# Optimization experiments

Measured on AMD Instinct MI355X. Metric: run time of the kernel, lower is better.

## Reference

```python
import jax, jax.numpy as jnp
import numpy as np

# OGB feature vocab sizes
ATOM_DIMS = [119, 4, 12, 12, 10, 6, 6, 2, 2]
BOND_DIMS = [5, 6, 2]
ATOM_OFF = np.concatenate([[0], np.cumsum(ATOM_DIMS)[:-1]]).astype(np.int32)
BOND_OFF = np.concatenate([[0], np.cumsum(BOND_DIMS)[:-1]]).astype(np.int32)
SCHEDULE_LEN = 5   # len(train_schedule) == len(eval_schedule)
NUM_GRAPHS = 12000
BN_EPS = 1e-5

N_NODES, N_EDGES, HIDDEN, NUM_TASKS = 300000, 600000, 128, 128


def setup_inputs() -> dict:
    key = jax.random.key(0)
    ks = jax.random.split(key, 16)
    x = jax.random.randint(ks[0], (N_NODES, 9), 0, 2, dtype=jnp.int32)
    edge_index = jax.random.randint(ks[1], (2, N_EDGES), 0, N_NODES, dtype=jnp.int32)
    edge_attr = jax.random.randint(ks[2], (N_EDGES, 3), 0, 2, dtype=jnp.int32)
    batch = jnp.sort(jax.random.randint(ks[3], (N_NODES,), 0, NUM_GRAPHS, dtype=jnp.int32))
    # learned parameters (embedding tables concatenated with offsets)
    atom_emb = jax.random.normal(ks[4], (sum(ATOM_DIMS), HIDDEN), jnp.float32) * 0.1
    bond_emb = jax.random.normal(ks[5], (sum(BOND_DIMS), HIDDEN), jnp.float32) * 0.1
    conv_W = jax.random.normal(ks[6], (HIDDEN, HIDDEN), jnp.float32) * (1.0 / np.sqrt(HIDDEN))
    conv_b = jnp.zeros((HIDDEN,), jnp.float32)
    root_emb = jax.random.normal(ks[7], (HIDDEN,), jnp.float32) * 0.1
    bn_gamma = jnp.ones((HIDDEN,), jnp.float32)
    bn_beta = jnp.zeros((HIDDEN,), jnp.float32)
    bn_mean = jnp.zeros((HIDDEN,), jnp.float32)   # running stats (eval mode)
    bn_var = jnp.ones((HIDDEN,), jnp.float32)
    lin_W = jax.random.normal(ks[8], (NUM_TASKS, HIDDEN), jnp.float32) * (1.0 / np.sqrt(HIDDEN))
    lin_b = jnp.zeros((NUM_TASKS,), jnp.float32)
    return {"x": x, "edge_index": edge_index, "edge_attr": edge_attr, "batch": batch,
            "atom_emb": atom_emb, "bond_emb": bond_emb, "conv_W": conv_W, "conv_b": conv_b,
            "root_emb": root_emb, "bn_gamma": bn_gamma, "bn_beta": bn_beta,
            "bn_mean": bn_mean, "bn_var": bn_var, "lin_W": lin_W, "lin_b": lin_b}


def reference(x, edge_index, edge_attr, batch, atom_emb, bond_emb, conv_W, conv_b,
              root_emb, bn_gamma, bn_beta, bn_mean, bn_var, lin_W, lin_b):
    N = x.shape[0]
    # AtomEncoder / BondEncoder: sum of per-feature embedding lookups
    h = atom_emb[x + jnp.asarray(ATOM_OFF, x.dtype)].sum(axis=1)            # [N, H]
    e = bond_emb[edge_attr + jnp.asarray(BOND_OFF, edge_attr.dtype)].sum(axis=1)  # [E, H]
    row, col = edge_index[0], edge_index[1]
    deg = jax.ops.segment_sum(jnp.ones_like(row, h.dtype), row, num_segments=N) + 1.0  # [N]
    dis = deg ** -0.5                                                        # deg >= 1, no inf
    norm = dis[row] * dis[col]                                               # [E]
    inv_std = bn_gamma / jnp.sqrt(bn_var + BN_EPS)
    for i in range(SCHEDULE_LEN):
        old = h
        z = h @ conv_W.T + conv_b                                            # [N, H]
        # message: norm * relu(x_j + edge_emb), aggregated at target (col) via scatter-add
        msg = norm[:, None] * jax.nn.relu(z[row] + e)                        # [E, H]
        agg = jax.ops.segment_sum(msg, col, num_segments=N)                  # [N, H]
        z = agg + jax.nn.relu(z + root_emb) / deg[:, None]                   # self-loop term
        z = jax.nn.relu(z)
        z = (z - bn_mean) * inv_std + bn_beta                                # BN (eval, running stats)
        # dropout: identity in eval mode
        # NOTE: faithful to source bug: smooth_fac is the loop index i, not schedule[i]
        h = i * old + (1 - i) * z
    # global mean pool over graphs
    counts = jax.ops.segment_sum(jnp.ones((N,), h.dtype), batch, num_segments=NUM_GRAPHS)
    pooled = jax.ops.segment_sum(h, batch, num_segments=NUM_GRAPHS) / jnp.maximum(counts, 1.0)[:, None]
    return pooled @ lin_W.T + lin_b                                          # [num_graphs, num_tasks]
```

## Files before the change

kernel.cpp:

```cpp
#include <hip/hip_runtime.h>

#define HID 128
#define AROWS 173

typedef __attribute__((ext_vector_type(8))) short short8;
typedef __attribute__((ext_vector_type(8))) unsigned short ushort8v;
typedef __attribute__((ext_vector_type(4))) float floatx4;
typedef __attribute__((ext_vector_type(4))) unsigned short ushort4v;

__device__ __forceinline__ unsigned short f2bf(float f) {
    unsigned u = __builtin_bit_cast(unsigned, f);
    u += 0x7FFF + ((u >> 16) & 1);
    return (unsigned short)(u >> 16);
}
__device__ __forceinline__ float bf2f(unsigned short s) {
    unsigned u = ((unsigned)s) << 16;
    return __builtin_bit_cast(float, u);
}

__global__ void fillrd_kernel(float* __restrict__ dis, int* __restrict__ indeg,
                              int* __restrict__ dhist, int N)
{
    int i = blockIdx.x * 256 + threadIdx.x;
    if (i < N) { dis[i] = 0.f; indeg[i] = 0; }
    if (blockIdx.x == 0 && threadIdx.x < 32) dhist[threadIdx.x] = 0;
}

__global__ void diag_kernel(float* __restrict__ out, long n, float val)
{
    long i = (long)blockIdx.x * blockDim.x + threadIdx.x;
    if (i < n) out[i] = val;
}

__global__ __launch_bounds__(256) void tables_kernel(
    const float* __restrict__ conv_W, unsigned short* __restrict__ Wb,
    const float* __restrict__ lin_W, unsigned short* __restrict__ linWb,
    const float* __restrict__ bond_emb, unsigned short* __restrict__ comb,
    const float* __restrict__ gamma, const float* __restrict__ beta,
    const float* __restrict__ mean, const float* __restrict__ var,
    float* __restrict__ bnsc, float* __restrict__ bnsh,
    const float* __restrict__ atom_emb, unsigned short* __restrict__ aeb)
{
    int blk = blockIdx.x;
    int tid = threadIdx.x;
    if (blk < 64) {
        int i = blk * 256 + tid;
        Wb[i] = f2bf(conv_W[i]);
    } else if (blk < 128) {
        int i = (blk - 64) * 256 + tid;
        linWb[i] = f2bf(lin_W[i]);
    } else if (blk < 158) {
        int i = (blk - 128) * 2 + (tid >> 7);
        int c = tid & 127;
        int a0 = i / 12, a1 = (i % 12) / 2, a2 = i % 2;
        comb[i * HID + c] = f2bf(bond_emb[a0 * HID + c] + bond_emb[(5 + a1) * HID + c]
                               + bond_emb[(11 + a2) * HID + c]);
    } else if (blk == 158) {
        if (tid < HID) {
            float sc = gamma[tid] * rsqrtf(var[tid] + 1e-5f);
            bnsc[tid] = sc;
            bnsh[tid] = beta[tid] - mean[tid] * sc;
        }
    } else {
        int i = (blk - 159) * 256 + tid;
        if (i < AROWS * HID) aeb[i] = f2bf(atom_emb[i]);
    }
}

__global__ void hist_kernel(const int* __restrict__ ei, float* __restrict__ dis,
                            int* __restrict__ indeg, int E)
{
    for (int e = blockIdx.x * blockDim.x + threadIdx.x; e < E; e += gridDim.x * blockDim.x) {
        atomicAdd(&dis[ei[e]], 1.f);
        atomicAdd(&indeg[ei[E + e]], 1);
    }
}

__global__ __launch_bounds__(256) void fdh_kernel(
    float* __restrict__ dis, const int* __restrict__ indeg,
    int* __restrict__ dhist, int N)
{
    __shared__ int lh[32];
    int tid = threadIdx.x;
    if (tid < 32) lh[tid] = 0;
    __syncthreads();
    int i = blockIdx.x * 256 + tid;
    if (i < N) {
        dis[i] = rsqrtf(dis[i] + 1.f);
        int d = indeg[i]; if (d > 31) d = 31;
        atomicAdd(&lh[d], 1);
    }
    __syncthreads();
    if (tid < 32 && lh[tid]) atomicAdd(&dhist[tid], lh[tid]);
}

__global__ void dscan_kernel(const int* __restrict__ dhist, int* __restrict__ dcur)
{
    if (threadIdx.x == 0) {
        int s = 0;
        for (int k = 0; k < 32; ++k) { dcur[k] = s; s += dhist[k]; }
    }
}

__global__ __launch_bounds__(256) void dperm_kernel(
    const int* __restrict__ indeg, int* __restrict__ dcur,
    int* __restrict__ perm, int* __restrict__ invperm, int N)
{
    __shared__ int lh[32];
    __shared__ int gb[32];
    int tid = threadIdx.x;
    if (tid < 32) lh[tid] = 0;
    __syncthreads();
    int n = blockIdx.x * 256 + tid;
    int rank = 0, d = 0;
    if (n < N) {
        d = indeg[n]; if (d > 31) d = 31;
        rank = atomicAdd(&lh[d], 1);
    }
    __syncthreads();
    if (tid < 32) gb[tid] = lh[tid] ? atomicAdd(&dcur[tid], lh[tid]) : 0;
    __syncthreads();
    if (n < N) {
        int slot = gb[d] + rank;
        perm[slot] = n;
        invperm[n] = slot;
    }
}

__global__ __launch_bounds__(256) void sbsum_kernel(
    const int* __restrict__ indeg, const int* __restrict__ perm,
    int* __restrict__ partial, int N)
{
    __shared__ int s[256];
    int tid = threadIdx.x;
    int i = blockIdx.x * 256 + tid;
    s[tid] = (i < N) ? indeg[perm[i]] : 0;
    __syncthreads();
    for (int d = 128; d > 0; d >>= 1) {
        if (tid < d) s[tid] += s[tid + d];
        __syncthreads();
    }
    if (tid == 0) partial[blockIdx.x] = s[0];
}

__global__ __launch_bounds__(256) void sscan1_kernel(
    const int* __restrict__ partial, int* __restrict__ offs,
    int* __restrict__ sptr, int B, int N)
{
    __shared__ int s[256];
    __shared__ int carry_s;
    int tid = threadIdx.x;
    if (tid == 0) carry_s = 0;
    __syncthreads();
    for (int base = 0; base < B; base += 256) {
        int i = base + tid;
        int v = (i < B) ? partial[i] : 0;
        s[tid] = v;
        __syncthreads();
        for (int d = 1; d < 256; d <<= 1) {
            int t = (tid >= d) ? s[tid - d] : 0;
            __syncthreads();
            s[tid] += t;
            __syncthreads();
        }
        int carry = carry_s;
        if (i < B) offs[i] = carry + s[tid] - v;
        __syncthreads();
        if (tid == 0) carry_s = carry + s[255];
        __syncthreads();
    }
    if (tid == 0) sptr[N] = carry_s;
}

__global__ __launch_bounds__(256) void sscan2_kernel(
    const int* __restrict__ indeg, const int* __restrict__ perm,
    const int* __restrict__ offs, int* __restrict__ sptr,
    int* __restrict__ scursor, int N)
{
    __shared__ int s[256];
    int tid = threadIdx.x;
    int i = blockIdx.x * 256 + tid;
    int v = (i < N) ? indeg[perm[i]] : 0;
    s[tid] = v;
    __syncthreads();
    for (int d = 1; d < 256; d <<= 1) {
        int t = (tid >= d) ? s[tid - d] : 0;
        __syncthreads();
        s[tid] += t;
        __syncthreads();
    }
    if (i < N) {
        int ex = offs[blockIdx.x] + s[tid] - v;
        sptr[i] = ex;
        scursor[i] = ex;
    }
}

__global__ void fillcsr_kernel(const int* __restrict__ ei, const int* __restrict__ attr,
                               const float* __restrict__ dis,
                               const int* __restrict__ invperm,
                               int* __restrict__ scursor,
                               int2* __restrict__ edata, const int* __restrict__ batch,
                               int* __restrict__ gptr, int E, int N, int G)
{
    for (int e = blockIdx.x * blockDim.x + threadIdx.x; e < E; e += gridDim.x * blockDim.x) {
        int r   = ei[e];
        int col = ei[E + e];
        int slot = invperm[col];
        int pos = atomicAdd(&scursor[slot], 1);
        int ci  = attr[e * 3] * 12 + attr[e * 3 + 1] * 2 + attr[e * 3 + 2];
        float nrm = dis[r] * dis[col];
        int2 ed;
        ed.x = r;
        ed.y = ci | ((int)f2bf(nrm) << 16);
        edata[pos] = ed;
    }
    for (int n = blockIdx.x * blockDim.x + threadIdx.x; n < N; n += gridDim.x * blockDim.x) {
        int b = batch[n];
        int bp = (n == 0) ? -1 : batch[n - 1];
        for (int g = bp + 1; g <= b; ++g) gptr[g] = n;
        if (n == N - 1)
            for (int g = b + 1; g <= G; ++g) gptr[g] = N;
    }
}

template<bool FIRST>
__global__ __launch_bounds__(256) void agg_kernel(
    const int* __restrict__ perm, const int* __restrict__ sptr,
    const int2* __restrict__ edata, const unsigned short* __restrict__ comb,
    const float* __restrict__ dis, const float* __restrict__ root,
    const float* __restrict__ bnsc, const float* __restrict__ bnsh,
    const unsigned short* __restrict__ zb, unsigned short* __restrict__ hb,
    float fi, int N)
{
    long slot = (long)blockIdx.x * 16 + (threadIdx.x >> 4);
    if (slot >= N) return;
    long n = perm[slot];
    int c = (threadIdx.x & 15) * 8;

    int jb = sptr[slot], je = sptr[slot + 1];

    ushort8v zv = *reinterpret_cast<const ushort8v*>(zb + n * HID + c);
    ushort8v hv;
    if constexpr (!FIRST) hv = *reinterpret_cast<const ushort8v*>(hb + n * HID + c);
    float di = dis[n];
    float rd = di * di;
    float acc[8];
#pragma unroll
    for (int j = 0; j < 8; ++j) acc[j] = fmaxf(bf2f(zv[j]) + root[c + j], 0.f) * rd;

    int j2 = jb;
    for (; j2 + 1 < je; j2 += 2) {
        int2 e0 = edata[j2];
        int2 e1 = edata[j2 + 1];
        ushort8v z0 = *reinterpret_cast<const ushort8v*>(zb + (long)e0.x * HID + c);
        ushort8v z1 = *reinterpret_cast<const ushort8v*>(zb + (long)e1.x * HID + c);
        ushort8v c0 = *reinterpret_cast<const ushort8v*>(comb + (e0.y & 0xFF) * HID + c);
        ushort8v c1 = *reinterpret_cast<const ushort8v*>(comb + (e1.y & 0xFF) * HID + c);
        float n0 = bf2f((unsigned short)(((unsigned)e0.y) >> 16));
        float n1 = bf2f((unsigned short)(((unsigned)e1.y) >> 16));
#pragma unroll
        for (int j = 0; j < 8; ++j) {
            acc[j] += fmaxf(bf2f(z0[j]) + bf2f(c0[j]), 0.f) * n0;
            acc[j] += fmaxf(bf2f(z1[j]) + bf2f(c1[j]), 0.f) * n1;
        }
    }
    if (j2 < je) {
        int2 e0 = edata[j2];
        ushort8v z0 = *reinterpret_cast<const ushort8v*>(zb + (long)e0.x * HID + c);
        ushort8v c0 = *reinterpret_cast<const ushort8v*>(comb + (e0.y & 0xFF) * HID + c);
        float n0 = bf2f((unsigned short)(((unsigned)e0.y) >> 16));
#pragma unroll
        for (int j = 0; j < 8; ++j)
            acc[j] += fmaxf(bf2f(z0[j]) + bf2f(c0[j]), 0.f) * n0;
    }

    ushort8v o;
#pragma unroll
    for (int j = 0; j < 8; ++j) {
        float t = fmaxf(acc[j], 0.f) * bnsc[c + j] + bnsh[c + j];
        float h;
        if constexpr (FIRST) h = t;
        else h = fi * bf2f(hv[j]) + (1.f - fi) * t;
        o[j] = f2bf(h);
    }
    *reinterpret_cast<ushort8v*>(hb + n * HID + c) = o;
}

__device__ __forceinline__ void gemm_from_lds(
    unsigned short (*hs)[132], const unsigned short* __restrict__ Wb,
    const float* __restrict__ bias, unsigned short* __restrict__ zb,
    long base, int N, int tid)
{
    int wave = tid >> 6;
    int lane = tid & 63;
    int l15 = lane & 15;
    int q = lane >> 4;
    int rowl0 = wave * 32;

    short8 a[2][4];
#pragma unroll
    for (int mt = 0; mt < 2; ++mt) {
        int rl = rowl0 + mt * 16 + l15;
#pragma unroll
        for (int kb = 0; kb < 4; ++kb)
            a[mt][kb] = *reinterpret_cast<const short8*>(&hs[rl][q * 8 + kb * 32]);
    }

    floatx4 acc[2][8];
#pragma unroll
    for (int mt = 0; mt < 2; ++mt)
#pragma unroll
        for (int nt = 0; nt < 8; ++nt) {
            floatx4 zz = {0.f, 0.f, 0.f, 0.f};
            acc[mt][nt] = zz;
        }

#pragma unroll
    for (int nt = 0; nt < 8; ++nt) {
        const unsigned short* bp = Wb + (nt * 16 + l15) * HID + q * 8;
#pragma unroll
        for (int kb = 0; kb < 4; ++kb) {
            short8 b = *reinterpret_cast<const short8*>(bp + kb * 32);
            acc[0][nt] = __builtin_amdgcn_mfma_f32_16x16x32_bf16(a[0][kb], b, acc[0][nt], 0, 0, 0);
            acc[1][nt] = __builtin_amdgcn_mfma_f32_16x16x32_bf16(a[1][kb], b, acc[1][nt], 0, 0, 0);
        }
    }

    float bi[8];
#pragma unroll
    for (int nt = 0; nt < 8; ++nt) bi[nt] = bias[nt * 16 + l15];

    __syncthreads();
#pragma unroll
    for (int mt = 0; mt < 2; ++mt)
#pragma unroll
        for (int r = 0; r < 4; ++r) {
            int lr = rowl0 + mt * 16 + q * 4 + r;
#pragma unroll
            for (int nt = 0; nt < 8; ++nt)
                hs[lr][l15 + 16 * nt] = f2bf(acc[mt][nt][r] + bi[nt]);
        }
    __syncthreads();

    int tr = tid >> 4;
    int tc = (tid & 15) * 8;
#pragma unroll
    for (int i = 0; i < 8; ++i) {
        int row = i * 16 + tr;
        long gr = base + row;
        if (gr < N) {
            ushort8v v = *reinterpret_cast<const ushort8v*>(&hs[row][tc]);
            *reinterpret_cast<ushort8v*>(zb + gr * HID + tc) = v;
        }
    }
}

__global__ __launch_bounds__(256) void egemm_kernel(
    const int* __restrict__ x, const unsigned short* __restrict__ aeb,
    const unsigned short* __restrict__ Wb, const float* __restrict__ bias,
    unsigned short* __restrict__ zb, int N)
{
    __shared__ unsigned short hs[64][132];
    __shared__ int xs[64 * 9];
    int tid = threadIdx.x;
    long base = (long)blockIdx.x * 64;
    const int OFF[9] = {0, 119, 123, 135, 147, 157, 163, 169, 171};

    int nb = (N - base < 64) ? (int)(N - base) : 64;
    int cnt = nb * 9;
    for (int i = tid; i < cnt; i += 256) xs[i] = x[base * 9 + i];
    __syncthreads();

    int sn = tid >> 4;
    int cc = (tid & 15) * 8;
#pragma unroll 1
    for (int s = 0; s < 4; ++s) {
        int lr = s * 16 + sn;
        ushort8v o;
        if (lr < nb) {
            float acc[8];
#pragma unroll
            for (int j = 0; j < 8; ++j) acc[j] = 0.f;
#pragma unroll
            for (int f = 0; f < 9; ++f) {
                int idx = xs[lr * 9 + f] + OFF[f];
                ushort8v v = *reinterpret_cast<const ushort8v*>(aeb + (long)idx * HID + cc);
#pragma unroll
                for (int j = 0; j < 8; ++j) acc[j] += bf2f(v[j]);
            }
#pragma unroll
            for (int j = 0; j < 8; ++j) o[j] = f2bf(acc[j]);
        } else {
            ushort8v z8 = {0, 0, 0, 0, 0, 0, 0, 0};
            o = z8;
        }
        *reinterpret_cast<ushort8v*>(&hs[lr][cc]) = o;
    }
    __syncthreads();

    int wave = tid >> 6;
    int lane = tid & 63;
    int l15 = lane & 15;
    int q = lane >> 4;
    int row0 = wave * 16;

    short8 a[4];
#pragma unroll
    for (int kb = 0; kb < 4; ++kb)
        a[kb] = *reinterpret_cast<const short8*>(&hs[row0 + l15][q * 8 + kb * 32]);

    floatx4 acc[8];
#pragma unroll
    for (int nt = 0; nt < 8; ++nt) {
        floatx4 zz = {0.f, 0.f, 0.f, 0.f};
        acc[nt] = zz;
    }
#pragma unroll
    for (int nt = 0; nt < 8; ++nt) {
        const unsigned short* bp = Wb + (nt * 16 + l15) * HID + q * 8;
#pragma unroll
        for (int kb = 0; kb < 4; ++kb) {
            short8 b = *reinterpret_cast<const short8*>(bp + kb * 32);
            acc[nt] = __builtin_amdgcn_mfma_f32_16x16x32_bf16(a[kb], b, acc[nt], 0, 0, 0);
        }
    }

    float bi[8];
#pragma unroll
    for (int nt = 0; nt < 8; ++nt) bi[nt] = bias[nt * 16 + l15];

#pragma unroll
    for (int r = 0; r < 4; ++r) {
        int lr = row0 + q * 4 + r;
#pragma unroll
        for (int nt = 0; nt < 8; ++nt)
            hs[lr][l15 + 16 * nt] = f2bf(acc[nt][r] + bi[nt]);
    }
    __syncthreads();

    int tr = tid >> 4;
    int tc = (tid & 15) * 8;
#pragma unroll
    for (int i = 0; i < 4; ++i) {
        int row = i * 16 + tr;
        long gr = base + row;
        if (gr < N) {
            ushort8v v = *reinterpret_cast<const ushort8v*>(&hs[row][tc]);
            *reinterpret_cast<ushort8v*>(zb + gr * HID + tc) = v;
        }
    }
}

__global__ __launch_bounds__(256) void gemm_kernel(
    const unsigned short* __restrict__ hb, const unsigned short* __restrict__ Wb,
    const float* __restrict__ bias, unsigned short* __restrict__ zb, int N)
{
    __shared__ unsigned short st[128][132];
    int tid = threadIdx.x;
    int wave = tid >> 6;
    int lane = tid & 63;
    int l15 = lane & 15;
    int q = lane >> 4;
    long base = (long)blockIdx.x * 128;
    long row0 = base + wave * 32;

#pragma unroll
    for (int mt = 0; mt < 2; ++mt) {
        long rl = row0 + mt * 16 + l15;
        if (rl > (long)N - 1) rl = (long)N - 1;
        const unsigned short* ap = hb + rl * HID + q * 8;
        int lrow = wave * 32 + mt * 16 + l15;
#pragma unroll
        for (int kb = 0; kb < 4; ++kb)
            *reinterpret_cast<ushort8v*>(&st[lrow][q * 8 + kb * 32]) =
                *reinterpret_cast<const ushort8v*>(ap + kb * 32);
    }
    __syncthreads();
    gemm_from_lds(st, Wb, bias, zb, base, N, tid);
}

__global__ __launch_bounds__(256) void linmm_kernel(
    const unsigned short* __restrict__ pb, const unsigned short* __restrict__ Wb,
    const float* __restrict__ bias, float* __restrict__ out, int G)
{
    int wave = threadIdx.x >> 6;
    int lane = threadIdx.x & 63;
    int l15 = lane & 15;
    int q = lane >> 4;
    long row0 = (long)blockIdx.x * 128 + wave * 32;

    short8 a[2][4];
#pragma unroll
    for (int mt = 0; mt < 2; ++mt) {
        long rl = row0 + mt * 16 + l15;
        if (rl > (long)G - 1) rl = (long)G - 1;
        const unsigned short* ap = pb + rl * HID + q * 8;
#pragma unroll
        for (int kb = 0; kb < 4; ++kb)
            a[mt][kb] = *reinterpret_cast<const short8*>(ap + kb * 32);
    }

    floatx4 acc[2][8];
#pragma unroll
    for (int mt = 0; mt < 2; ++mt)
#pragma unroll
        for (int nt = 0; nt < 8; ++nt) {
            floatx4 zz = {0.f, 0.f, 0.f, 0.f};
            acc[mt][nt] = zz;
        }

#pragma unroll
    for (int nt = 0; nt < 8; ++nt) {
        const unsigned short* bp = Wb + (nt * 16 + l15) * HID + q * 8;
#pragma unroll
        for (int kb = 0; kb < 4; ++kb) {
            short8 b = *reinterpret_cast<const short8*>(bp + kb * 32);
            acc[0][nt] = __builtin_amdgcn_mfma_f32_16x16x32_bf16(a[0][kb], b, acc[0][nt], 0, 0, 0);
            acc[1][nt] = __builtin_amdgcn_mfma_f32_16x16x32_bf16(a[1][kb], b, acc[1][nt], 0, 0, 0);
        }
    }

    float bi[8];
#pragma unroll
    for (int nt = 0; nt < 8; ++nt) bi[nt] = bias[nt * 16 + l15];

#pragma unroll
    for (int mt = 0; mt < 2; ++mt)
#pragma unroll
        for (int r = 0; r < 4; ++r) {
            long rr = row0 + mt * 16 + q * 4 + r;
            if (rr < G) {
                float* op = out + rr * HID + l15;
#pragma unroll
                for (int nt = 0; nt < 8; ++nt)
                    op[nt * 16] = acc[mt][nt][r] + bi[nt];
            }
        }
}

__global__ __launch_bounds__(256) void pool_kernel(
    const unsigned short* __restrict__ hb, const int* __restrict__ gptr,
    unsigned short* __restrict__ pb, int G)
{
    int g = blockIdx.x;
    if (g >= G) return;
    int tid = threadIdx.x;
    int sub = tid >> 5;
    int c = (tid & 31) * 4;
    int lo = gptr[g], hi = gptr[g + 1];
    floatx4 s = {0.f, 0.f, 0.f, 0.f};
    for (int n = lo + sub; n < hi; n += 8) {
        ushort4v hv = *reinterpret_cast<const ushort4v*>(hb + (long)n * HID + c);
#pragma unroll
        for (int j = 0; j < 4; ++j) s[j] += bf2f(hv[j]);
    }
    __shared__ float ps[8][HID];
    *reinterpret_cast<floatx4*>(&ps[sub][c]) = s;
    __syncthreads();
    if (tid < HID) {
        float sum = 0.f;
#pragma unroll
        for (int k = 0; k < 8; ++k) sum += ps[k][tid];
        float cnt = (hi > lo) ? (float)(hi - lo) : 1.f;
        pb[(long)g * HID + tid] = f2bf(sum / cnt);
    }
}

extern "C" void kernel_launch(void* const* d_in, const int* in_sizes, int n_in,
                              void* d_out, int out_size, void* d_ws, size_t ws_size,
                              hipStream_t stream)
{
    const int* x          = (const int*)d_in[0];
    const int* ei         = (const int*)d_in[1];
    const int* attr       = (const int*)d_in[2];
    const int* batch      = (const int*)d_in[3];
    const float* atom_emb = (const float*)d_in[4];
    const float* bond_emb = (const float*)d_in[5];
    const float* conv_W   = (const float*)d_in[6];
    const float* conv_b   = (const float*)d_in[7];
    const float* root     = (const float*)d_in[8];
    const float* gamma    = (const float*)d_in[9];
    const float* beta     = (const float*)d_in[10];
    const float* mean     = (const float*)d_in[11];
    const float* var      = (const float*)d_in[12];
    const float* lin_W    = (const float*)d_in[13];
    const float* lin_b    = (const float*)d_in[14];
    float* out = (float*)d_out;

    const int N = in_sizes[0] / 9;
    const int E = in_sizes[1] / 2;
    const int G = out_size / HID;
    const int B = (N + 255) / 256;

    auto al = [](size_t b) { return (b + 255) & ~(size_t)255; };
    const size_t need =
        al((size_t)N * HID * 2) +
        al((size_t)N * HID * 2) +
        al((size_t)(N + 1) * 4) +
        al((size_t)E * 8) +
        al((size_t)N * 4) +
        al((size_t)N * 4) +
        al((size_t)N * 4) +
        al((size_t)N * 4) +
        al((size_t)2048 * 4) * 2 +
        al((size_t)(G + 1) * 4) +
        al((size_t)(G + 128) * HID * 2) +
        al((size_t)60 * HID * 2) +
        al((size_t)HID * 4) * 2 +
        al((size_t)HID * HID * 2) * 2 +
        al((size_t)AROWS * HID * 2) +
        al(32 * 4) * 2;

    if (ws_size < need || B > 2048) {
        float v = (B > 2048) ? 3000.f : (1000.f + (float)(ws_size >> 20));
        long n = (long)out_size;
        diag_kernel<<<(int)((n + 255) / 256), 256, 0, stream>>>(out, n, v);
        return;
    }

    char* wsp = (char*)d_ws;
    size_t used = 0;
    auto alloc = [&](size_t bytes) { char* p = wsp + used; used += al(bytes); return p; };
    unsigned short* hb = (unsigned short*)alloc((size_t)N * HID * 2);
    unsigned short* zb = (unsigned short*)alloc((size_t)N * HID * 2);
    int* sptr     = (int*)alloc((size_t)(N + 1) * 4);
    int2* edata   = (int2*)alloc((size_t)E * 8);
    int* indeg    = (int*)alloc((size_t)N * 4);
    int* perm     = (int*)alloc((size_t)N * 4);
    int* invperm  = (int*)alloc((size_t)N * 4);
    int* scursor  = (int*)alloc((size_t)N * 4);
    int* partial  = (int*)alloc((size_t)2048 * 4);
    int* offs     = (int*)alloc((size_t)2048 * 4);
    int* gptr     = (int*)alloc((size_t)(G + 1) * 4);
    unsigned short* pb = (unsigned short*)alloc((size_t)(G + 128) * HID * 2);
    float* dis    = (float*)pb;
    unsigned short* comb = (unsigned short*)alloc((size_t)60 * HID * 2);
    float* bnsc   = (float*)alloc((size_t)HID * 4);
    float* bnsh   = (float*)alloc((size_t)HID * 4);
    unsigned short* Wb    = (unsigned short*)alloc((size_t)HID * HID * 2);
    unsigned short* linWb = (unsigned short*)alloc((size_t)HID * HID * 2);
    unsigned short* aeb   = (unsigned short*)alloc((size_t)AROWS * HID * 2);
    int* dhist    = (int*)alloc(32 * 4);
    int* dcur     = (int*)alloc(32 * 4);

    fillrd_kernel<<<B, 256, 0, stream>>>(dis, indeg, dhist, N);
    tables_kernel<<<246, 256, 0, stream>>>(conv_W, Wb, lin_W, linWb, bond_emb, comb,
                                           gamma, beta, mean, var, bnsc, bnsh,
                                           atom_emb, aeb);
    hist_kernel<<<1024, 256, 0, stream>>>(ei, dis, indeg, E);
    fdh_kernel<<<B, 256, 0, stream>>>(dis, indeg, dhist, N);
    dscan_kernel<<<1, 64, 0, stream>>>(dhist, dcur);
    dperm_kernel<<<B, 256, 0, stream>>>(indeg, dcur, perm, invperm, N);
    sbsum_kernel<<<B, 256, 0, stream>>>(indeg, perm, partial, N);
    sscan1_kernel<<<1, 256, 0, stream>>>(partial, offs, sptr, B, N);
    sscan2_kernel<<<B, 256, 0, stream>>>(indeg, perm, offs, sptr, scursor, N);
    fillcsr_kernel<<<1024, 256, 0, stream>>>(ei, attr, dis, invperm, scursor, edata,
                                             batch, gptr, E, N, G);

    const int egemm_blocks = (N + 63) / 64;
    const int gemm_blocks  = (N + 127) / 128;
    const int agg_blocks   = (N + 15) / 16;
    egemm_kernel<<<egemm_blocks, 256, 0, stream>>>(x, aeb, Wb, conv_b, zb, N);
    agg_kernel<true ><<<agg_blocks, 256, 0, stream>>>(perm, sptr, edata, comb, dis,
            root, bnsc, bnsh, zb, hb, 0.f, N);
    const float fis[3] = {2.f, 3.f, 4.f};
    for (int t = 0; t < 3; ++t) {
        gemm_kernel<<<gemm_blocks, 256, 0, stream>>>(hb, Wb, conv_b, zb, N);
        agg_kernel<false><<<agg_blocks, 256, 0, stream>>>(perm, sptr, edata, comb, dis,
                root, bnsc, bnsh, zb, hb, fis[t], N);
    }

    pool_kernel<<<G, 256, 0, stream>>>(hb, gptr, pb, G);
    linmm_kernel<<<(G + 127) / 128, 256, 0, stream>>>(pb, linWb, lin_b, out, G);
}
```

Baseline: 749.1 us.

## Process two nodes per thread group in aggregation and enlarge embed-GEMM tiles

```diff
diff --git a/kernel.cpp b/kernel.cpp
--- a/kernel.cpp
+++ b/kernel.cpp
@@ -224,6 +224,18 @@
     }
 }
 
+__device__ __forceinline__ void edge_acc(
+    int2 e, const unsigned short* __restrict__ zb,
+    const unsigned short* __restrict__ comb, int c, float* acc)
+{
+    ushort8v z = *reinterpret_cast<const ushort8v*>(zb + (long)e.x * HID + c);
+    ushort8v cb = *reinterpret_cast<const ushort8v*>(comb + (e.y & 0xFF) * HID + c);
+    float nr = bf2f((unsigned short)(((unsigned)e.y) >> 16));
+#pragma unroll
+    for (int j = 0; j < 8; ++j)
+        acc[j] += fmaxf(bf2f(z[j]) + bf2f(cb[j]), 0.f) * nr;
+}
+
 template<bool FIRST>
 __global__ __launch_bounds__(256) void agg_kernel(
     const int* __restrict__ perm, const int* __restrict__ sptr,
@@ -233,58 +245,84 @@
     const unsigned short* __restrict__ zb, unsigned short* __restrict__ hb,
     float fi, int N)
 {
-    long slot = (long)blockIdx.x * 16 + (threadIdx.x >> 4);
-    if (slot >= N) return;
-    long n = perm[slot];
+    long s0 = (long)blockIdx.x * 32 + (threadIdx.x >> 4);
+    if (s0 >= N) return;
+    long s1 = s0 + 16;
+    bool has1 = (s1 < N);
     int c = (threadIdx.x & 15) * 8;
 
-    int jb = sptr[slot], je = sptr[slot + 1];
-
-    ushort8v zv = *reinterpret_cast<const ushort8v*>(zb + n * HID + c);
-    ushort8v hv;
-    if constexpr (!FIRST) hv = *reinterpret_cast<const ushort8v*>(hb + n * HID + c);
-    float di = dis[n];
-    float rd = di * di;
-    float acc[8];
-#pragma unroll
-    for (int j = 0; j < 8; ++j) acc[j] = fmaxf(bf2f(zv[j]) + root[c + j], 0.f) * rd;
-
-    int j2 = jb;
-    for (; j2 + 1 < je; j2 += 2) {
-        int2 e0 = edata[j2];
-        int2 e1 = edata[j2 + 1];
-        ushort8v z0 = *reinterpret_cast<const ushort8v*>(zb + (long)e0.x * HID + c);
-        ushort8v z1 = *reinterpret_cast<const ushort8v*>(zb + (long)e1.x * HID + c);
-        ushort8v c0 = *reinterpret_cast<const ushort8v*>(comb + (e0.y & 0xFF) * HID + c);
-        ushort8v c1 = *reinterpret_cast<const ushort8v*>(comb + (e1.y & 0xFF) * HID + c);
-        float n0 = bf2f((unsigned short)(((unsigned)e0.y) >> 16));
-        float n1 = bf2f((unsigned short)(((unsigned)e1.y) >> 16));
-#pragma unroll
-        for (int j = 0; j < 8; ++j) {
-            acc[j] += fmaxf(bf2f(z0[j]) + bf2f(c0[j]), 0.f) * n0;
-            acc[j] += fmaxf(bf2f(z1[j]) + bf2f(c1[j]), 0.f) * n1;
-        }
-    }
-    if (j2 < je) {
-        int2 e0 = edata[j2];
-        ushort8v z0 = *reinterpret_cast<const ushort8v*>(zb + (long)e0.x * HID + c);
-        ushort8v c0 = *reinterpret_cast<const ushort8v*>(comb + (e0.y & 0xFF) * HID + c);
-        float n0 = bf2f((unsigned short)(((unsigned)e0.y) >> 16));
-#pragma unroll
-        for (int j = 0; j < 8; ++j)
-            acc[j] += fmaxf(bf2f(z0[j]) + bf2f(c0[j]), 0.f) * n0;
-    }
-
-    ushort8v o;
+    long n0 = perm[s0];
+    long n1 = has1 ? (long)perm[s1] : n0;
+    int jb0 = sptr[s0], je0 = sptr[s0 + 1];
+    int jb1 = 0, je1 = 0;
+    if (has1) { jb1 = sptr[s1]; je1 = sptr[s1 + 1]; }
+
+    float rt[8], sc[8], sh[8];
 #pragma unroll
     for (int j = 0; j < 8; ++j) {
-        float t = fmaxf(acc[j], 0.f) * bnsc[c + j] + bnsh[c + j];
-        float h;
-        if constexpr (FIRST) h = t;
-        else h = fi * bf2f(hv[j]) + (1.f - fi) * t;
-        o[j] = f2bf(h);
-    }
-    *reinterpret_cast<ushort8v*>(hb + n * HID + c) = o;
+        rt[j] = root[c + j]; sc[j] = bnsc[c + j]; sh[j] = bnsh[c + j];
+    }
+
+    ushort8v zv0 = *reinterpret_cast<const ushort8v*>(zb + n0 * HID + c);
+    ushort8v zv1 = has1 ? *reinterpret_cast<const ushort8v*>(zb + n1 * HID + c) : zv0;
+    ushort8v hv0, hv1;
+    if constexpr (!FIRST) {
+        hv0 = *reinterpret_cast<const ushort8v*>(hb + n0 * HID + c);
+        if (has1) hv1 = *reinterpret_cast<const ushort8v*>(hb + n1 * HID + c);
+    }
+    float d0 = dis[n0], d1 = dis[n1];
+    float rd0 = d0 * d0, rd1 = d1 * d1;
+
+    float acc0[8], acc1[8];
+#pragma unroll
+    for (int j = 0; j < 8; ++j) {
+        acc0[j] = fmaxf(bf2f(zv0[j]) + rt[j], 0.f) * rd0;
+        acc1[j] = fmaxf(bf2f(zv1[j]) + rt[j], 0.f) * rd1;
+    }
+
+    int j0 = jb0, j1 = jb1;
+    while (j0 + 1 < je0 && j1 + 1 < je1) {
+        int2 ea = edata[j0];
+        int2 eb = edata[j0 + 1];
+        int2 ec = edata[j1];
+        int2 ed = edata[j1 + 1];
+        edge_acc(ea, zb, comb, c, acc0);
+        edge_acc(eb, zb, comb, c, acc0);
+        edge_acc(ec, zb, comb, c, acc1);
+        edge_acc(ed, zb, comb, c, acc1);
+        j0 += 2; j1 += 2;
+    }
+    for (; j0 + 1 < je0; j0 += 2) {
+        int2 ea = edata[j0];
+        int2 eb = edata[j0 + 1];
+        edge_acc(ea, zb, comb, c, acc0);
+        edge_acc(eb, zb, comb, c, acc0);
+    }
+    if (j0 < je0) edge_acc(edata[j0], zb, comb, c, acc0);
+    for (; j1 + 1 < je1; j1 += 2) {
+        int2 ec = edata[j1];
+        int2 ed = edata[j1 + 1];
+        edge_acc(ec, zb, comb, c, acc1);
+        edge_acc(ed, zb, comb, c, acc1);
+    }
+    if (j1 < je1) edge_acc(edata[j1], zb, comb, c, acc1);
+
+    ushort8v o0, o1;
+#pragma unroll
+    for (int j = 0; j < 8; ++j) {
+        float t0 = fmaxf(acc0[j], 0.f) * sc[j] + sh[j];
+        float t1 = fmaxf(acc1[j], 0.f) * sc[j] + sh[j];
+        float h0, h1;
+        if constexpr (FIRST) { h0 = t0; h1 = t1; }
+        else {
+            h0 = fi * bf2f(hv0[j]) + (1.f - fi) * t0;
+            h1 = fi * bf2f(hv1[j]) + (1.f - fi) * t1;
+        }
+        o0[j] = f2bf(h0);
+        o1[j] = f2bf(h1);
+    }
+    *reinterpret_cast<ushort8v*>(hb + n0 * HID + c) = o0;
+    if (has1) *reinterpret_cast<ushort8v*>(hb + n1 * HID + c) = o1;
 }
 
 __device__ __forceinline__ void gemm_from_lds(
@@ -361,13 +399,13 @@
     const unsigned short* __restrict__ Wb, const float* __restrict__ bias,
     unsigned short* __restrict__ zb, int N)
 {
-    __shared__ unsigned short hs[64][132];
-    __shared__ int xs[64 * 9];
-    int tid = threadIdx.x;
-    long base = (long)blockIdx.x * 64;
+    __shared__ unsigned short hs[128][132];
+    __shared__ int xs[128 * 9];
+    int tid = threadIdx.x;
+    long base = (long)blockIdx.x * 128;
     const int OFF[9] = {0, 119, 123, 135, 147, 157, 163, 169, 171};
 
-    int nb = (N - base < 64) ? (int)(N - base) : 64;
+    int nb = (N - base < 128) ? (int)(N - base) : 128;
     int cnt = nb * 9;
     for (int i = tid; i < cnt; i += 256) xs[i] = x[base * 9 + i];
     __syncthreads();
@@ -375,7 +413,7 @@
     int sn = tid >> 4;
     int cc = (tid & 15) * 8;
 #pragma unroll 1
-    for (int s = 0; s < 4; ++s) {
+    for (int s = 0; s < 8; ++s) {
         int lr = s * 16 + sn;
         ushort8v o;
         if (lr < nb) {
@@ -399,57 +437,7 @@
     }
     __syncthreads();
 
-    int wave = tid >> 6;
-    int lane = tid & 63;
-    int l15 = lane & 15;
-    int q = lane >> 4;
-    int row0 = wave * 16;
-
-    short8 a[4];
-#pragma unroll
-    for (int kb = 0; kb < 4; ++kb)
-        a[kb] = *reinterpret_cast<const short8*>(&hs[row0 + l15][q * 8 + kb * 32]);
-
-    floatx4 acc[8];
-#pragma unroll
-    for (int nt = 0; nt < 8; ++nt) {
-        floatx4 zz = {0.f, 0.f, 0.f, 0.f};
-        acc[nt] = zz;
-    }
-#pragma unroll
-    for (int nt = 0; nt < 8; ++nt) {
-        const unsigned short* bp = Wb + (nt * 16 + l15) * HID + q * 8;
-#pragma unroll
-        for (int kb = 0; kb < 4; ++kb) {
-            short8 b = *reinterpret_cast<const short8*>(bp + kb * 32);
-            acc[nt] = __builtin_amdgcn_mfma_f32_16x16x32_bf16(a[kb], b, acc[nt], 0, 0, 0);
-        }
-    }
-
-    float bi[8];
-#pragma unroll
-    for (int nt = 0; nt < 8; ++nt) bi[nt] = bias[nt * 16 + l15];
-
-#pragma unroll
-    for (int r = 0; r < 4; ++r) {
-        int lr = row0 + q * 4 + r;
-#pragma unroll
-        for (int nt = 0; nt < 8; ++nt)
-            hs[lr][l15 + 16 * nt] = f2bf(acc[nt][r] + bi[nt]);
-    }
-    __syncthreads();
-
-    int tr = tid >> 4;
-    int tc = (tid & 15) * 8;
-#pragma unroll
-    for (int i = 0; i < 4; ++i) {
-        int row = i * 16 + tr;
-        long gr = base + row;
-        if (gr < N) {
-            ushort8v v = *reinterpret_cast<const ushort8v*>(&hs[row][tc]);
-            *reinterpret_cast<ushort8v*>(zb + gr * HID + tc) = v;
-        }
-    }
+    gemm_from_lds(hs, Wb, bias, zb, base, N, tid);
 }
 
 __global__ __launch_bounds__(256) void gemm_kernel(
@@ -658,10 +646,9 @@
     fillcsr_kernel<<<1024, 256, 0, stream>>>(ei, attr, dis, invperm, scursor, edata,
                                              batch, gptr, E, N, G);
 
-    const int egemm_blocks = (N + 63) / 64;
-    const int gemm_blocks  = (N + 127) / 128;
-    const int agg_blocks   = (N + 15) / 16;
-    egemm_kernel<<<egemm_blocks, 256, 0, stream>>>(x, aeb, Wb, conv_b, zb, N);
+    const int gemm_blocks = (N + 127) / 128;
+    const int agg_blocks  = (N + 31) / 32;
+    egemm_kernel<<<gemm_blocks, 256, 0, stream>>>(x, aeb, Wb, conv_b, zb, N);
     agg_kernel<true ><<<agg_blocks, 256, 0, stream>>>(perm, sptr, edata, comb, dis,
             root, bnsc, bnsh, zb, hb, 0.f, N);
     const float fis[3] = {2.f, 3.f, 4.f};
```

Result: faster. 726.6 us (-3.0%).
